# Performance work log

Measured on AMD Instinct MI355X. Metric: run time of the kernel, lower is better.

Reference implementation:

```python
import jax, jax.numpy as jnp
import numpy as np

B, C, H, W = 8, 64, 128, 128
G, DGPG = 4, 1
GD = G * DGPG          # total deformable groups = 4
COUT = 64
KH = KW = 3
K = KH * KW            # 9 kernel locations
PAD = STR = DIL = 1
HO, WO = 128, 128      # same padding, stride 1
OFFSET_SCALE = 1.0
CDG = C // GD          # channels per deformable group = 16
CPG = C // G           # input channels per conv group = 16
KOFF = 7
POFF = 3


def dwconv7(x, w, b):
    # depthwise 7x7 conv, groups == channels; w: [C,1,7,7]
    y = jax.lax.conv_general_dilated(
        x, w, window_strides=(1, 1), padding=[(POFF, POFF), (POFF, POFF)],
        feature_group_count=C, dimension_numbers=('NCHW', 'OIHW', 'NCHW'))
    return y + b[None, :, None, None]


def gn1(x, g, b):
    # GroupNorm with a single group: normalize over (C,H,W) per sample
    m = x.mean(axis=(1, 2, 3), keepdims=True)
    v = x.var(axis=(1, 2, 3), keepdims=True)
    return (x - m) * jax.lax.rsqrt(v + 1e-5) * g[None, :, None, None] + b[None, :, None, None]


def pw(x, w, b):
    # 1x1 conv; w: [O, C]
    return jnp.einsum('bchw,oc->bohw', x, w) + b[None, :, None, None]


def setup_inputs() -> dict:
    key = jax.random.key(0)
    ks = jax.random.split(key, 8)
    s = 0.02
    return {
        'x': jax.random.normal(ks[0], (B, C, H, W), jnp.float32),
        'w_dw_off': jax.random.normal(ks[1], (C, 1, KOFF, KOFF), jnp.float32) * s,
        'b_dw_off': jnp.zeros((C,), jnp.float32),
        'gn_off_g': jnp.ones((C,), jnp.float32),
        'gn_off_b': jnp.zeros((C,), jnp.float32),
        'w_pw_off': jax.random.normal(ks[2], (GD * K * 2, C), jnp.float32) * s,
        'b_pw_off': jnp.zeros((GD * K * 2,), jnp.float32),
        'w_dw_m': jax.random.normal(ks[3], (C, 1, KOFF, KOFF), jnp.float32) * s,
        'b_dw_m': jnp.zeros((C,), jnp.float32),
        'gn_m_g': jnp.ones((C,), jnp.float32),
        'gn_m_b': jnp.zeros((C,), jnp.float32),
        'w_pw_m': jax.random.normal(ks[4], (GD * K, C), jnp.float32) * s,
        'b_pw_m': jnp.zeros((GD * K,), jnp.float32),
        'weight': jax.random.normal(ks[5], (COUT, CPG, KH, KW), jnp.float32) * s,
        'bias': jax.random.normal(ks[6], (COUT,), jnp.float32) * s,
    }


def _deform_conv(x, offset, mask, weight, bias):
    # offset: [B, GD, K, 2, HO, WO] (y, x); mask: [B, GD, K, HO, WO] (softmaxed)
    ky, kx = jnp.meshgrid(jnp.arange(KH), jnp.arange(KW), indexing='ij')
    ky = ky.reshape(K).astype(x.dtype)
    kx = kx.reshape(K).astype(x.dtype)
    oy = jnp.arange(HO, dtype=x.dtype)
    ox = jnp.arange(WO, dtype=x.dtype)
    base_y = oy[None, :] * STR - PAD + ky[:, None] * DIL   # [K, HO]
    base_x = ox[None, :] * STR - PAD + kx[:, None] * DIL   # [K, WO]
    py = base_y[None, None, :, :, None] + offset[:, :, :, 0] * OFFSET_SCALE  # [B,GD,K,HO,WO]
    px = base_x[None, None, :, None, :] + offset[:, :, :, 1] * OFFSET_SCALE

    x_flat = x.reshape(B, GD, CDG, H * W)
    y0 = jnp.floor(py)
    x0 = jnp.floor(px)
    wy = py - y0
    wx = px - x0

    def gather(yi, xi):
        valid = ((yi >= 0) & (yi < H) & (xi >= 0) & (xi < W)).astype(x.dtype)
        yc = jnp.clip(yi, 0, H - 1).astype(jnp.int32)
        xc = jnp.clip(xi, 0, W - 1).astype(jnp.int32)
        idx = (yc * W + xc).reshape(B, GD, 1, K * HO * WO)
        v = jnp.take_along_axis(x_flat, idx, axis=3).reshape(B, GD, CDG, K, HO, WO)
        return v * valid[:, :, None]

    v = (gather(y0, x0) * ((1 - wy) * (1 - wx))[:, :, None]
         + gather(y0, x0 + 1) * ((1 - wy) * wx)[:, :, None]
         + gather(y0 + 1, x0) * (wy * (1 - wx))[:, :, None]
         + gather(y0 + 1, x0 + 1) * (wy * wx)[:, :, None])
    v = v * mask[:, :, None]                               # modulated samples
    v = v.reshape(B, G, CPG, K, HO, WO)
    wg = weight.reshape(G, COUT // G, CPG, K)
    out = jnp.einsum('bgckhw,gock->bgohw', v, wg).reshape(B, COUT, HO, WO)
    return out + bias[None, :, None, None]


def reference(x, w_dw_off, b_dw_off, gn_off_g, gn_off_b, w_pw_off, b_pw_off,
              w_dw_m, b_dw_m, gn_m_g, gn_m_b, w_pw_m, b_pw_m, weight, bias):
    off = pw(gn1(dwconv7(x, w_dw_off, b_dw_off), gn_off_g, gn_off_b), w_pw_off, b_pw_off)
    m = pw(gn1(dwconv7(x, w_dw_m, b_dw_m), gn_m_g, gn_m_b), w_pw_m, b_pw_m)
    offset = off.reshape(B, GD, K, 2, HO, WO)
    mask = jax.nn.softmax(m.reshape(B, GD, K, HO, WO), axis=2)  # attn over kernel points
    return _deform_conv(x, offset, mask, weight, bias)
```

## Files before the change

kernel.cpp:

```cpp
#include <hip/hip_runtime.h>
#include <hip/hip_fp16.h>
#include <math.h>

#define HW     16384
#define IMG_H  128
#define IMG_W  128

typedef _Float16 f16x2 __attribute__((ext_vector_type(2)));
typedef __fp16 fp16v2 __attribute__((ext_vector_type(2)));
typedef _Float16 f16x4 __attribute__((ext_vector_type(4)));
typedef float f32x4 __attribute__((ext_vector_type(4)));

#define OFF_T2    ((size_t)0)
#define OFF_XT    ((size_t)8388608)
#define OFF_WT    ((size_t)12582912)
#define OFF_PART  ((size_t)12599040)
#define OFF_AD    ((size_t)12631808)
#define OFF_WB    ((size_t)19711744)
#define OFF_WDW2  ((size_t)19716352)
#define OFF_WPK   ((size_t)19719936)
#define OFF_DC    ((size_t)19775232)

__global__ void k_prep(const float* __restrict__ wpw_off,
                       const float* __restrict__ wpw_m,
                       const float* __restrict__ wdef,
                       const float* __restrict__ wdwo,
                       const float* __restrict__ wdwm,
                       float* __restrict__ ws) {
    int i = blockIdx.x * 256 + threadIdx.x;
    if (i < 6912) {
        int c = i / 108, o = i % 108;
        ws[OFF_WT + i] = (o < 72) ? wpw_off[o * 64 + c] : wpw_m[(o - 72) * 64 + c];
    } else if (i < 9216) {
        int j = i - 6912;
        int lane = j & 63;
        int gt = j >> 6;
        int tap = gt % 9, g = gt / 9;
        int oc = lane & 15, qh = lane >> 4;
        union { ushort h[4]; uint2 u; } pk;
#pragma unroll
        for (int jj = 0; jj < 4; ++jj) {
            float wv = wdef[((g * 16 + oc) * 16 + (4 * qh + jj)) * 9 + tap];
            pk.h[jj] = __half_as_ushort(__float2half(wv));
        }
        ((uint2*)(ws + OFF_WB))[j] = pk.u;
    } else if (i < 12800) {
        int j = i - 9216;
        int q = j & 3;
        int r = j >> 2;
        int dy = r % 7;
        int cv = (r / 7) & 1;
        int c = r / 14;
        const float* src = cv ? wdwm : wdwo;
        int dx0 = q * 2;
        float w0 = src[c * 49 + dy * 7 + dx0];
        float w1 = (dx0 + 1 < 7) ? src[c * 49 + dy * 7 + dx0 + 1] : 0.f;
        union { __half h[2]; uint u; } pk;
        pk.h[0] = __float2half(w0);
        pk.h[1] = __float2half(w1);
        ((uint*)(ws + OFF_WDW2))[j] = pk.u;
    }
}

__global__ __launch_bounds__(256) void k_trans(const float* __restrict__ x,
                                               __half* __restrict__ xT) {
    int n = blockIdx.x * 256 + threadIdx.x;
    int p = n & (HW - 1);
    int bg = n >> 14;
    const float* src = x + (size_t)bg * 16 * HW + p;
    union { __half2 h2[8]; uint4 u[2]; } pk;
#pragma unroll
    for (int i = 0; i < 8; ++i) {
        float a = src[(size_t)(2 * i) * HW];
        float bq = src[(size_t)(2 * i + 1) * HW];
        pk.h2[i] = __halves2half2(__float2half(a), __float2half(bq));
    }
    uint4* dst = (uint4*)(xT + (size_t)n * 16);
    dst[0] = pk.u[0];
    dst[1] = pk.u[1];
}

__global__ __launch_bounds__(256) void k_dw(const float* __restrict__ x,
                                            const float* __restrict__ bdwo,
                                            const float* __restrict__ bdwm,
                                            const uint* __restrict__ wdw2,
                                            uint2* __restrict__ t2p,
                                            float* __restrict__ partial) {
    int bid = blockIdx.x;
    int b = bid >> 9;
    int c2 = (bid >> 4) & 31;
    int stripe = (bid & 15) * 8;
    int t = threadIdx.x;
    int cb = t & 31;
    int row = stripe + (t >> 5);
    int c0 = c2 * 2;

    float vo[2][4], vm[2][4];
    float s1o = 0.f, s2o = 0.f, s1m = 0.f, s2m = 0.f;
    union CV { fp16v2 v; f16x2 h; };
    union WU { uint u; f16x2 h; };

#pragma unroll
    for (int ch = 0; ch < 2; ++ch) {
        int c = c0 + ch;
        const float4* pl = (const float4*)(x + ((size_t)(b * 64 + c)) * HW);
        const uint* wp = wdw2 + c * 56;
        float acco[4] = {0.f, 0.f, 0.f, 0.f};
        float accm[4] = {0.f, 0.f, 0.f, 0.f};
#pragma unroll
        for (int dy = 0; dy < 7; ++dy) {
            int iy = row - 3 + dy;
            if (iy >= 0 && iy < IMG_H) {
                const float4* prow = pl + iy * 32;
                float4 f4 = prow[cb];
                float4 f4m = prow[cb == 0 ? 0 : cb - 1];
                float4 f4p = prow[cb == 31 ? 31 : cb + 1];
                bool le = (cb == 0), re = (cb == 31);
                float v[11];
                v[0] = le ? 0.f : f4m.y;
                v[1] = le ? 0.f : f4m.z;
                v[2] = le ? 0.f : f4m.w;
                v[3] = f4.x; v[4] = f4.y; v[5] = f4.z; v[6] = f4.w;
                v[7] = re ? 0.f : f4p.x;
                v[8] = re ? 0.f : f4p.y;
                v[9] = re ? 0.f : f4p.z;
                v[10] = re ? 0.f : f4p.w;
                f16x2 hp[10];
#pragma unroll
                for (int d = 0; d < 10; ++d) {
                    CV cv;
                    cv.v = __builtin_amdgcn_cvt_pkrtz(v[d], v[d + 1]);
                    hp[d] = cv.h;
                }
#pragma unroll
                for (int cc = 0; cc < 4; ++cc) {
                    WU w0, w1, w2, w3, u0, u1, u2, u3;
                    w0.u = wp[dy * 4 + 0]; w1.u = wp[dy * 4 + 1];
                    w2.u = wp[dy * 4 + 2]; w3.u = wp[dy * 4 + 3];
                    u0.u = wp[28 + dy * 4 + 0]; u1.u = wp[28 + dy * 4 + 1];
                    u2.u = wp[28 + dy * 4 + 2]; u3.u = wp[28 + dy * 4 + 3];
                    float ao = acco[cc], am = accm[cc];
                    ao = __builtin_amdgcn_fdot2(hp[cc],     w0.h, ao, false);
                    ao = __builtin_amdgcn_fdot2(hp[cc + 2], w1.h, ao, false);
                    ao = __builtin_amdgcn_fdot2(hp[cc + 4], w2.h, ao, false);
                    ao = __builtin_amdgcn_fdot2(hp[cc + 6], w3.h, ao, false);
                    am = __builtin_amdgcn_fdot2(hp[cc],     u0.h, am, false);
                    am = __builtin_amdgcn_fdot2(hp[cc + 2], u1.h, am, false);
                    am = __builtin_amdgcn_fdot2(hp[cc + 4], u2.h, am, false);
                    am = __builtin_amdgcn_fdot2(hp[cc + 6], u3.h, am, false);
                    acco[cc] = ao; accm[cc] = am;
                }
            }
        }
        float bo = bdwo[c], bm = bdwm[c];
#pragma unroll
        for (int cc = 0; cc < 4; ++cc) {
            float o_ = acco[cc] + bo, m_ = accm[cc] + bm;
            vo[ch][cc] = o_; vm[ch][cc] = m_;
            s1o += o_; s2o += o_ * o_; s1m += m_; s2m += m_ * m_;
        }
    }

    union { uint2 u2[4]; uint4 u4[2]; } ot;
#pragma unroll
    for (int cc = 0; cc < 4; ++cc) {
        ot.u2[cc].x = (uint)__half_as_ushort(__float2half(vo[0][cc])) |
                      ((uint)__half_as_ushort(__float2half(vo[1][cc])) << 16);
        ot.u2[cc].y = (uint)__half_as_ushort(__float2half(vm[0][cc])) |
                      ((uint)__half_as_ushort(__float2half(vm[1][cc])) << 16);
    }
    uint4* dst = (uint4*)(t2p + ((size_t)(b * 32 + c2) * HW + row * IMG_W + cb * 4));
    dst[0] = ot.u4[0];
    dst[1] = ot.u4[1];

#pragma unroll
    for (int d = 32; d; d >>= 1) {
        s1o += __shfl_down(s1o, d);
        s2o += __shfl_down(s2o, d);
        s1m += __shfl_down(s1m, d);
        s2m += __shfl_down(s2m, d);
    }
    __shared__ float red[4][4];
    if ((t & 63) == 0) {
        int w = t >> 6;
        red[w][0] = s1o; red[w][1] = s2o; red[w][2] = s1m; red[w][3] = s2m;
    }
    __syncthreads();
    if (t < 4) {
        float v = red[0][t] + red[1][t] + red[2][t] + red[3][t];
        partial[(size_t)bid * 4 + t] = v;
    }
}

__global__ __launch_bounds__(256) void k_fin(const float* __restrict__ partial,
                      const float* __restrict__ gog, const float* __restrict__ gob,
                      const float* __restrict__ gmg, const float* __restrict__ gmb,
                      float* __restrict__ ad) {
    int b = blockIdx.x, t = threadIdx.x;
    const float4* pp = (const float4*)partial + (size_t)b * 512;
    float4 s = make_float4(0.f, 0.f, 0.f, 0.f);
#pragma unroll
    for (int i = 0; i < 2; ++i) {
        float4 v = pp[t + i * 256];
        s.x += v.x; s.y += v.y; s.z += v.z; s.w += v.w;
    }
#pragma unroll
    for (int d = 32; d; d >>= 1) {
        s.x += __shfl_down(s.x, d);
        s.y += __shfl_down(s.y, d);
        s.z += __shfl_down(s.z, d);
        s.w += __shfl_down(s.w, d);
    }
    __shared__ float red[4][4];
    if ((t & 63) == 0) {
        int w = t >> 6;
        red[w][0] = s.x; red[w][1] = s.y; red[w][2] = s.z; red[w][3] = s.w;
    }
    __syncthreads();
    if (t < 64) {
        float s1o = red[0][0] + red[1][0] + red[2][0] + red[3][0];
        float s2o = red[0][1] + red[1][1] + red[2][1] + red[3][1];
        float s1m = red[0][2] + red[1][2] + red[2][2] + red[3][2];
        float s2m = red[0][3] + red[1][3] + red[2][3] + red[3][3];
        int c = t;
        const float invN = 1.f / 1048576.f;
        float m_o = s1o * invN;
        float v_o = s2o * invN - m_o * m_o;
        float i_o = rsqrtf(v_o + 1e-5f);
        float m_m = s1m * invN;
        float v_m = s2m * invN - m_m * m_m;
        float i_m = rsqrtf(v_m + 1e-5f);
        float a_o = i_o * gog[c];
        float d_o = gob[c] - m_o * a_o;
        float a_m = i_m * gmg[c];
        float d_m = gmb[c] - m_m * a_m;
        ((float4*)ad)[b * 64 + c] = make_float4(a_o, d_o, a_m, d_m);
    }
}

__global__ __launch_bounds__(256) void k_fold(const float* __restrict__ wT,
                                              const float* __restrict__ ad,
                                              const float* __restrict__ bpo,
                                              const float* __restrict__ bpm,
                                              uint* __restrict__ wpk,
                                              float* __restrict__ dconst) {
    int b = blockIdx.x, t = threadIdx.x;
    const float* adb = ad + b * 256;
    for (int i = t; i < 3456; i += 256) {
        int o27 = i % 27;
        int c2 = (i / 27) & 31;
        int g = i / (27 * 32);
        int c0 = c2 * 2, c1 = c0 + 1;
        float w0, w1;
        if (o27 < 18) {
            int o = g * 18 + o27;
            w0 = adb[c0 * 4 + 0] * wT[c0 * 108 + o];
            w1 = adb[c1 * 4 + 0] * wT[c1 * 108 + o];
        } else {
            int o = 72 + g * 9 + (o27 - 18);
            w0 = adb[c0 * 4 + 2] * wT[c0 * 108 + o];
            w1 = adb[c1 * 4 + 2] * wT[c1 * 108 + o];
        }
        wpk[(size_t)b * 3456 + i] =
            (uint)__half_as_ushort(__float2half(w0)) |
            ((uint)__half_as_ushort(__float2half(w1)) << 16);
    }
    if (t < 108) {
        float s = (t < 72) ? bpo[t] : bpm[t - 72];
        for (int c = 0; c < 64; ++c) {
            float d = (t < 72) ? adb[c * 4 + 1] : adb[c * 4 + 3];
            s = fmaf(d, wT[c * 108 + t], s);
        }
        dconst[b * 108 + t] = s;
    }
}

__global__ __launch_bounds__(256, 4) void k_gthf(const uint2* __restrict__ t2p,
                                                 const uint* __restrict__ wpk,
                                                 const float* __restrict__ dconst,
                                                 const __half* __restrict__ xT,
                                                 const uint2* __restrict__ wb,
                                                 const float* __restrict__ bias,
                                                 float* __restrict__ out) {
    __shared__ union SMem {
        struct {
            uint4 xsA[506];
            uint4 xsB[506];
            uint4 shv[768];
        } s;
        float shout[4864];
    } sm;

    int tid = threadIdx.x;
    int bid = blockIdx.x;
    int bg = bid >> 6;
    int tile = bid & 63;
    int tr = tile >> 3, tc = tile & 7;
    int r0 = tr * 16, c0 = tc * 16;
    int g = bg & 3, b = bg >> 2;
    int wr0 = r0 - 3, wc0 = c0 - 3;

    const __half* xg = xT + (size_t)bg * HW * 16;

#pragma unroll
    for (int it = 0; it < 2; ++it) {
        int idx = tid + it * 256;
        if (idx < 484) {
            int ly = idx / 22, lx = idx - ly * 22;
            int sr = wr0 + ly; sr = sr < 0 ? 0 : (sr > 127 ? 127 : sr);
            int sc = wc0 + lx; sc = sc < 0 ? 0 : (sc > 127 ? 127 : sc);
            const uint4* src = (const uint4*)(xg + (size_t)(sr * IMG_W + sc) * 16);
            sm.s.xsA[ly * 23 + lx] = src[0];
            sm.s.xsB[ly * 23 + lx] = src[1];
        }
    }

    int row = r0 + (tid >> 4), col = c0 + (tid & 15);
    int p = row * IMG_W + col;
    int lane = tid & 63, wv = tid >> 6;
    int m_idx = lane & 15, q_idx = lane >> 4;

    const float* dc = dconst + b * 108;
    float facc[18], macc[9];
#pragma unroll
    for (int o = 0; o < 18; ++o) facc[o] = dc[g * 18 + o];
#pragma unroll
    for (int o = 0; o < 9; ++o) macc[o] = dc[72 + g * 9 + o];

    const uint2* tp = t2p + (size_t)b * 32 * HW + p;
    const uint* wgp = wpk + ((size_t)(b * 4 + g)) * 32 * 27;
    union WU { uint u; f16x2 h; };
#pragma unroll 8
    for (int c2 = 0; c2 < 32; ++c2) {
        uint2 pk = tp[(size_t)c2 * HW];
        WU ho, hm;
        ho.u = pk.x; hm.u = pk.y;
        const uint* wr = wgp + c2 * 27;
#pragma unroll
        for (int o = 0; o < 18; ++o) {
            WU w; w.u = wr[o];
            facc[o] = __builtin_amdgcn_fdot2(ho.h, w.h, facc[o], false);
        }
#pragma unroll
        for (int o = 0; o < 9; ++o) {
            WU w; w.u = wr[18 + o];
            macc[o] = __builtin_amdgcn_fdot2(hm.h, w.h, macc[o], false);
        }
    }
    {
        float mx = macc[0];
#pragma unroll
        for (int k = 1; k < 9; ++k) mx = fmaxf(mx, macc[k]);
        float s = 0.f;
#pragma unroll
        for (int k = 0; k < 9; ++k) {
            float e = __expf(macc[k] - mx);
            macc[k] = e;
            s += e;
        }
        float inv = 1.f / s;
#pragma unroll
        for (int k = 0; k < 9; ++k) macc[k] *= inv;
    }

    const uint2* wbp = wb + (size_t)(g * 9) * 64 + lane;
    f16x4 bfr[9];
    union BU { uint2 u; f16x4 h; };
#pragma unroll
    for (int k = 0; k < 9; ++k) { BU t; t.u = wbp[k * 64]; bfr[k] = t.h; }

    __syncthreads();

    uint4* shvw = sm.s.shv + tid * 3;
    const _Float16* shvh = (const _Float16*)sm.s.shv;

    f32x4 acc[4];
#pragma unroll
    for (int s = 0; s < 4; ++s) acc[s] = (f32x4){0.f, 0.f, 0.f, 0.f};

#pragma unroll
    for (int k = 0; k < 9; ++k) {
        float mk = macc[k];
        float py = (float)(row + k / 3 - 1) + facc[k * 2 + 0];
        float px = (float)(col + k % 3 - 1) + facc[k * 2 + 1];
        float y0f = floorf(py), x0f = floorf(px);
        float wy = py - y0f, wx = px - x0f;
        int iy0 = (int)y0f, ix0 = (int)x0f;
        int iy1 = iy0 + 1, ix1 = ix0 + 1;
        float fy0 = (iy0 >= 0 && iy0 < IMG_H) ? (1.f - wy) : 0.f;
        float fy1 = (iy1 >= 0 && iy1 < IMG_H) ? wy : 0.f;
        float fx0 = (ix0 >= 0 && ix0 < IMG_W) ? (1.f - wx) : 0.f;
        float fx1 = (ix1 >= 0 && ix1 < IMG_W) ? wx : 0.f;
        __half2 f00h = __float2half2_rn(fy0 * fx0 * mk);
        __half2 f01h = __float2half2_rn(fy0 * fx1 * mk);
        __half2 f10h = __float2half2_rn(fy1 * fx0 * mk);
        __half2 f11h = __float2half2_rn(fy1 * fx1 * mk);
        int ly0 = iy0 - wr0; ly0 = ly0 < 0 ? 0 : (ly0 > 21 ? 21 : ly0);
        int ly1 = iy1 - wr0; ly1 = ly1 < 0 ? 0 : (ly1 > 21 ? 21 : ly1);
        int lx0 = ix0 - wc0; lx0 = lx0 < 0 ? 0 : (lx0 > 21 ? 21 : lx0);
        int lx1 = ix1 - wc0; lx1 = lx1 < 0 ? 0 : (lx1 > 21 ? 21 : lx1);
        int i00 = ly0 * 23 + lx0, i01 = ly0 * 23 + lx1;
        int i10 = ly1 * 23 + lx0, i11 = ly1 * 23 + lx1;
        union Q8 { uint4 u[2]; __half2 h2[8]; };
        Q8 q00, q01, q10, q11;
        q00.u[0] = sm.s.xsA[i00]; q00.u[1] = sm.s.xsB[i00];
        q01.u[0] = sm.s.xsA[i01]; q01.u[1] = sm.s.xsB[i01];
        q10.u[0] = sm.s.xsA[i10]; q10.u[1] = sm.s.xsB[i10];
        q11.u[0] = sm.s.xsA[i11]; q11.u[1] = sm.s.xsB[i11];
        union V8 { __half2 h2[4]; uint4 u; };
        V8 pa, pb;
#pragma unroll
        for (int i = 0; i < 4; ++i) {
            __half2 vh = __hmul2(f00h, q00.h2[i]);
            vh = __hfma2(f01h, q01.h2[i], vh);
            vh = __hfma2(f10h, q10.h2[i], vh);
            vh = __hfma2(f11h, q11.h2[i], vh);
            pa.h2[i] = vh;
        }
#pragma unroll
        for (int i = 4; i < 8; ++i) {
            __half2 vh = __hmul2(f00h, q00.h2[i]);
            vh = __hfma2(f01h, q01.h2[i], vh);
            vh = __hfma2(f10h, q10.h2[i], vh);
            vh = __hfma2(f11h, q11.h2[i], vh);
            pb.h2[i - 4] = vh;
        }
        shvw[0] = pa.u;
        shvw[1] = pb.u;
#pragma unroll
        for (int s = 0; s < 4; ++s) {
            f16x4 af = *(const f16x4*)(shvh +
                        ((size_t)wv * 64 + s * 16 + m_idx) * 24 + q_idx * 4);
            acc[s] = __builtin_amdgcn_mfma_f32_16x16x16f16(af, bfr[k], acc[s], 0, 0, 0);
        }
    }

    __syncthreads();

#pragma unroll
    for (int s = 0; s < 4; ++s)
#pragma unroll
        for (int j = 0; j < 4; ++j)
            sm.shout[(wv * 64 + s * 16 + 4 * q_idx + j) * 19 + m_idx] = acc[s][j];

    float* outp = out + ((size_t)b * 64 + g * 16) * HW + p;
#pragma unroll
    for (int o = 0; o < 16; ++o)
        outp[(size_t)o * HW] = sm.shout[tid * 19 + o] + bias[g * 16 + o];
}

extern "C" void kernel_launch(void* const* d_in, const int* in_sizes, int n_in,
                              void* d_out, int out_size, void* d_ws, size_t ws_size,
                              hipStream_t stream) {
    const float* x        = (const float*)d_in[0];
    const float* w_dw_off = (const float*)d_in[1];
    const float* b_dw_off = (const float*)d_in[2];
    const float* gn_off_g = (const float*)d_in[3];
    const float* gn_off_b = (const float*)d_in[4];
    const float* w_pw_off = (const float*)d_in[5];
    const float* b_pw_off = (const float*)d_in[6];
    const float* w_dw_m   = (const float*)d_in[7];
    const float* b_dw_m   = (const float*)d_in[8];
    const float* gn_m_g   = (const float*)d_in[9];
    const float* gn_m_b   = (const float*)d_in[10];
    const float* w_pw_m   = (const float*)d_in[11];
    const float* b_pw_m   = (const float*)d_in[12];
    const float* weight   = (const float*)d_in[13];
    const float* bias     = (const float*)d_in[14];

    float* ws = (float*)d_ws;
    uint2* t2p    = (uint2*)(ws + OFF_T2);
    __half* xT    = (__half*)(ws + OFF_XT);
    float* wT     = ws + OFF_WT;
    float* part   = ws + OFF_PART;
    float* adb    = ws + OFF_AD;
    const uint2* wb = (const uint2*)(ws + OFF_WB);
    const uint* wdw2 = (const uint*)(ws + OFF_WDW2);
    uint* wpk     = (uint*)(ws + OFF_WPK);
    float* dconst = ws + OFF_DC;

    k_prep<<<50, 256, 0, stream>>>(w_pw_off, w_pw_m, weight, w_dw_off, w_dw_m, ws);
    k_trans<<<2048, 256, 0, stream>>>(x, xT);
    k_dw<<<4096, 256, 0, stream>>>(x, b_dw_off, b_dw_m, wdw2, t2p, part);
    k_fin<<<8, 256, 0, stream>>>(part, gn_off_g, gn_off_b, gn_m_g, gn_m_b, adb);
    k_fold<<<8, 256, 0, stream>>>(wT, adb, b_pw_off, b_pw_m, wpk, dconst);
    k_gthf<<<2048, 256, 0, stream>>>(t2p, wpk, dconst, xT, wb, bias, (float*)d_out);
}
```

Baseline: 103.6 us.

## Compute offset/mask pointwise projection with MFMA instead of per-thread fdot2

Replaces the per-pixel fdot2 loop that produced the 18 offset and 9 mask logits with 16x16x16 fp16 MFMA tiles. k_fold now packs the GN-folded pointwise weights directly into MFMA B-fragment layout, with zero padding up to 32 and 16 outputs. The activations are staged through a per-wave LDS slab to form A fragments, and the accumulators are transposed back through LDS to per-pixel registers. This cuts the scalar ALU dot-product work in the fused gather kernel, at the cost of more LDS traffic and footprint. The offsets are also rounded to fp16 before the bias is added, which costs some accuracy.

```diff
diff --git a/kernel.cpp b/kernel.cpp
--- a/kernel.cpp
+++ b/kernel.cpp
@@ -18,8 +18,9 @@
 #define OFF_AD    ((size_t)12631808)
 #define OFF_WB    ((size_t)19711744)
 #define OFF_WDW2  ((size_t)19716352)
-#define OFF_WPK   ((size_t)19719936)
-#define OFF_DC    ((size_t)19775232)
+#define OFF_WBO   ((size_t)19719936)
+#define OFF_WBM   ((size_t)19752704)
+#define OFF_DC    ((size_t)19769088)
 
 __global__ void k_prep(const float* __restrict__ wpw_off,
                        const float* __restrict__ wpw_m,
@@ -242,28 +243,39 @@
                                               const float* __restrict__ ad,
                                               const float* __restrict__ bpo,
                                               const float* __restrict__ bpm,
-                                              uint* __restrict__ wpk,
+                                              uint2* __restrict__ wbo,
+                                              uint2* __restrict__ wbm,
                                               float* __restrict__ dconst) {
     int b = blockIdx.x, t = threadIdx.x;
     const float* adb = ad + b * 256;
-    for (int i = t; i < 3456; i += 256) {
-        int o27 = i % 27;
-        int c2 = (i / 27) & 31;
-        int g = i / (27 * 32);
-        int c0 = c2 * 2, c1 = c0 + 1;
-        float w0, w1;
-        if (o27 < 18) {
-            int o = g * 18 + o27;
-            w0 = adb[c0 * 4 + 0] * wT[c0 * 108 + o];
-            w1 = adb[c1 * 4 + 0] * wT[c1 * 108 + o];
-        } else {
-            int o = 72 + g * 9 + (o27 - 18);
-            w0 = adb[c0 * 4 + 2] * wT[c0 * 108 + o];
-            w1 = adb[c1 * 4 + 2] * wT[c1 * 108 + o];
-        }
-        wpk[(size_t)b * 3456 + i] =
-            (uint)__half_as_ushort(__float2half(w0)) |
-            ((uint)__half_as_ushort(__float2half(w1)) << 16);
+    for (int i = t; i < 2048; i += 256) {
+        int lane = i & 63;
+        int f = i >> 6;
+        int g = f >> 3, kk = (f >> 1) & 3, nf = f & 1;
+        int n = lane & 15, q = lane >> 4;
+        int out = nf * 16 + n;
+        union { ushort h[4]; uint2 u; } pk;
+#pragma unroll
+        for (int jj = 0; jj < 4; ++jj) {
+            int ch = kk * 16 + 4 * q + jj;
+            float w = (out < 18) ? adb[ch * 4 + 0] * wT[ch * 108 + g * 18 + out] : 0.f;
+            pk.h[jj] = __half_as_ushort(__float2half(w));
+        }
+        wbo[((size_t)(b * 4) + g) * 8 * 64 + (size_t)(kk * 2 + nf) * 64 + lane] = pk.u;
+    }
+    for (int i = t; i < 1024; i += 256) {
+        int lane = i & 63;
+        int f = i >> 6;
+        int g = f >> 2, kk = f & 3;
+        int n = lane & 15, q = lane >> 4;
+        union { ushort h[4]; uint2 u; } pk;
+#pragma unroll
+        for (int jj = 0; jj < 4; ++jj) {
+            int ch = kk * 16 + 4 * q + jj;
+            float w = (n < 9) ? adb[ch * 4 + 2] * wT[ch * 108 + 72 + g * 9 + n] : 0.f;
+            pk.h[jj] = __half_as_ushort(__float2half(w));
+        }
+        wbm[((size_t)(b * 4) + g) * 4 * 64 + (size_t)kk * 64 + lane] = pk.u;
     }
     if (t < 108) {
         float s = (t < 72) ? bpo[t] : bpm[t - 72];
@@ -276,7 +288,8 @@
 }
 
 __global__ __launch_bounds__(256, 4) void k_gthf(const uint2* __restrict__ t2p,
-                                                 const uint* __restrict__ wpk,
+                                                 const uint2* __restrict__ wbo,
+                                                 const uint2* __restrict__ wbm,
                                                  const float* __restrict__ dconst,
                                                  const __half* __restrict__ xT,
                                                  const uint2* __restrict__ wb,
@@ -286,7 +299,7 @@
         struct {
             uint4 xsA[506];
             uint4 xsB[506];
-            uint4 shv[768];
+            uint  slab[5120];
         } s;
         float shout[4864];
     } sm;
@@ -320,133 +333,187 @@
     int lane = tid & 63, wv = tid >> 6;
     int m_idx = lane & 15, q_idx = lane >> 4;
 
+    union BU { uint2 u; f16x4 h; };
+
+    const uint2* wboP = wbo + ((size_t)(b * 4) + g) * 8 * 64 + lane;
+    const uint2* wbmP = wbm + ((size_t)(b * 4) + g) * 4 * 64 + lane;
+    f16x4 bO[8], bM[4];
+#pragma unroll
+    for (int i = 0; i < 8; ++i) { BU t; t.u = wboP[i * 64]; bO[i] = t.h; }
+#pragma unroll
+    for (int i = 0; i < 4; ++i) { BU t; t.u = wbmP[i * 64]; bM[i] = t.h; }
+
+    const uint2* wbp = wb + (size_t)(g * 9) * 64 + lane;
+    f16x4 bfr[9];
+#pragma unroll
+    for (int k = 0; k < 9; ++k) { BU t; t.u = wbp[k * 64]; bfr[k] = t.h; }
+
+    uint* aslab = sm.s.slab + wv * 1280;
+    const uint2* tp = t2p + (size_t)b * 32 * HW + p;
+
+    f32x4 accO0[4], accO1[4], accM[4];
+#pragma unroll
+    for (int s = 0; s < 4; ++s) {
+        accO0[s] = (f32x4){0.f, 0.f, 0.f, 0.f};
+        accO1[s] = (f32x4){0.f, 0.f, 0.f, 0.f};
+        accM[s]  = (f32x4){0.f, 0.f, 0.f, 0.f};
+    }
+
+#pragma unroll
+    for (int kk = 0; kk < 4; ++kk) {
+        uint2 v[8];
+#pragma unroll
+        for (int j = 0; j < 8; ++j) v[j] = tp[(size_t)(kk * 8 + j) * HW];
+        uint* rowp = aslab + lane * 20;
+        ((uint4*)rowp)[0] = make_uint4(v[0].x, v[1].x, v[2].x, v[3].x);
+        ((uint4*)rowp)[1] = make_uint4(v[4].x, v[5].x, v[6].x, v[7].x);
+        ((uint4*)(rowp + 8))[0] = make_uint4(v[0].y, v[1].y, v[2].y, v[3].y);
+        ((uint4*)(rowp + 8))[1] = make_uint4(v[4].y, v[5].y, v[6].y, v[7].y);
+#pragma unroll
+        for (int s = 0; s < 4; ++s) {
+            const uint* pr = aslab + (s * 16 + m_idx) * 20 + 2 * q_idx;
+            BU ao, am;
+            ao.u = *(const uint2*)pr;
+            am.u = *(const uint2*)(pr + 8);
+            accO0[s] = __builtin_amdgcn_mfma_f32_16x16x16f16(ao.h, bO[kk * 2 + 0], accO0[s], 0, 0, 0);
+            accO1[s] = __builtin_amdgcn_mfma_f32_16x16x16f16(ao.h, bO[kk * 2 + 1], accO1[s], 0, 0, 0);
+            accM[s]  = __builtin_amdgcn_mfma_f32_16x16x16f16(am.h, bM[kk], accM[s], 0, 0, 0);
+        }
+    }
+
     const float* dc = dconst + b * 108;
-    float facc[18], macc[9];
-#pragma unroll
-    for (int o = 0; o < 18; ++o) facc[o] = dc[g * 18 + o];
-#pragma unroll
-    for (int o = 0; o < 9; ++o) macc[o] = dc[72 + g * 9 + o];
-
-    const uint2* tp = t2p + (size_t)b * 32 * HW + p;
-    const uint* wgp = wpk + ((size_t)(b * 4 + g)) * 32 * 27;
-    union WU { uint u; f16x2 h; };
-#pragma unroll 8
-    for (int c2 = 0; c2 < 32; ++c2) {
-        uint2 pk = tp[(size_t)c2 * HW];
-        WU ho, hm;
-        ho.u = pk.x; hm.u = pk.y;
-        const uint* wr = wgp + c2 * 27;
-#pragma unroll
-        for (int o = 0; o < 18; ++o) {
-            WU w; w.u = wr[o];
-            facc[o] = __builtin_amdgcn_fdot2(ho.h, w.h, facc[o], false);
-        }
-#pragma unroll
-        for (int o = 0; o < 9; ++o) {
-            WU w; w.u = wr[18 + o];
-            macc[o] = __builtin_amdgcn_fdot2(hm.h, w.h, macc[o], false);
-        }
-    }
+
+#pragma unroll
+    for (int s = 0; s < 4; ++s)
+#pragma unroll
+        for (int j = 0; j < 4; ++j) {
+            int px = s * 16 + 4 * q_idx + j;
+            union { __half2 h2; uint u; } pk;
+            pk.h2 = __halves2half2(__float2half(accO0[s][j]),
+                                   __float2half(accO1[s][j]));
+            aslab[px * 20 + m_idx] = pk.u;
+        }
+    float facc[18];
     {
+        const uint4* dr = (const uint4*)(aslab + lane * 20);
+        uint4 d0 = dr[0], d1 = dr[1], d2 = dr[2], d3 = dr[3];
+        uint du[16] = {d0.x, d0.y, d0.z, d0.w, d1.x, d1.y, d1.z, d1.w,
+                       d2.x, d2.y, d2.z, d2.w, d3.x, d3.y, d3.z, d3.w};
+        union { uint u; __half2 h2; } cv;
+#pragma unroll
+        for (int i = 0; i < 16; ++i) {
+            cv.u = du[i];
+            float2 f = __half22float2(cv.h2);
+            facc[i] = f.x + dc[g * 18 + i];
+            if (i < 2) facc[16 + i] = f.y + dc[g * 18 + 16 + i];
+        }
+    }
+
+    {
+        float* fsl = (float*)aslab;
+#pragma unroll
+        for (int s = 0; s < 4; ++s)
+#pragma unroll
+            for (int j = 0; j < 4; ++j) {
+                int px = s * 16 + 4 * q_idx + j;
+                fsl[px * 20 + m_idx] = accM[s][j];
+            }
+        float macc[9];
+#pragma unroll
+        for (int k = 0; k < 9; ++k) macc[k] = fsl[lane * 20 + k] + dc[72 + g * 9 + k];
         float mx = macc[0];
 #pragma unroll
         for (int k = 1; k < 9; ++k) mx = fmaxf(mx, macc[k]);
-        float s = 0.f;
+        float ssum = 0.f;
 #pragma unroll
         for (int k = 0; k < 9; ++k) {
             float e = __expf(macc[k] - mx);
             macc[k] = e;
-            s += e;
-        }
-        float inv = 1.f / s;
-#pragma unroll
-        for (int k = 0; k < 9; ++k) macc[k] *= inv;
-    }
-
-    const uint2* wbp = wb + (size_t)(g * 9) * 64 + lane;
-    f16x4 bfr[9];
-    union BU { uint2 u; f16x4 h; };
-#pragma unroll
-    for (int k = 0; k < 9; ++k) { BU t; t.u = wbp[k * 64]; bfr[k] = t.h; }
-
-    __syncthreads();
-
-    uint4* shvw = sm.s.shv + tid * 3;
-    const _Float16* shvh = (const _Float16*)sm.s.shv;
-
-    f32x4 acc[4];
-#pragma unroll
-    for (int s = 0; s < 4; ++s) acc[s] = (f32x4){0.f, 0.f, 0.f, 0.f};
-
-#pragma unroll
-    for (int k = 0; k < 9; ++k) {
-        float mk = macc[k];
-        float py = (float)(row + k / 3 - 1) + facc[k * 2 + 0];
-        float px = (float)(col + k % 3 - 1) + facc[k * 2 + 1];
-        float y0f = floorf(py), x0f = floorf(px);
-        float wy = py - y0f, wx = px - x0f;
-        int iy0 = (int)y0f, ix0 = (int)x0f;
-        int iy1 = iy0 + 1, ix1 = ix0 + 1;
-        float fy0 = (iy0 >= 0 && iy0 < IMG_H) ? (1.f - wy) : 0.f;
-        float fy1 = (iy1 >= 0 && iy1 < IMG_H) ? wy : 0.f;
-        float fx0 = (ix0 >= 0 && ix0 < IMG_W) ? (1.f - wx) : 0.f;
-        float fx1 = (ix1 >= 0 && ix1 < IMG_W) ? wx : 0.f;
-        __half2 f00h = __float2half2_rn(fy0 * fx0 * mk);
-        __half2 f01h = __float2half2_rn(fy0 * fx1 * mk);
-        __half2 f10h = __float2half2_rn(fy1 * fx0 * mk);
-        __half2 f11h = __float2half2_rn(fy1 * fx1 * mk);
-        int ly0 = iy0 - wr0; ly0 = ly0 < 0 ? 0 : (ly0 > 21 ? 21 : ly0);
-        int ly1 = iy1 - wr0; ly1 = ly1 < 0 ? 0 : (ly1 > 21 ? 21 : ly1);
-        int lx0 = ix0 - wc0; lx0 = lx0 < 0 ? 0 : (lx0 > 21 ? 21 : lx0);
-        int lx1 = ix1 - wc0; lx1 = lx1 < 0 ? 0 : (lx1 > 21 ? 21 : lx1);
-        int i00 = ly0 * 23 + lx0, i01 = ly0 * 23 + lx1;
-        int i10 = ly1 * 23 + lx0, i11 = ly1 * 23 + lx1;
-        union Q8 { uint4 u[2]; __half2 h2[8]; };
-        Q8 q00, q01, q10, q11;
-        q00.u[0] = sm.s.xsA[i00]; q00.u[1] = sm.s.xsB[i00];
-        q01.u[0] = sm.s.xsA[i01]; q01.u[1] = sm.s.xsB[i01];
-        q10.u[0] = sm.s.xsA[i10]; q10.u[1] = sm.s.xsB[i10];
-        q11.u[0] = sm.s.xsA[i11]; q11.u[1] = sm.s.xsB[i11];
-        union V8 { __half2 h2[4]; uint4 u; };
-        V8 pa, pb;
-#pragma unroll
-        for (int i = 0; i < 4; ++i) {
-            __half2 vh = __hmul2(f00h, q00.h2[i]);
-            vh = __hfma2(f01h, q01.h2[i], vh);
-            vh = __hfma2(f10h, q10.h2[i], vh);
-            vh = __hfma2(f11h, q11.h2[i], vh);
-            pa.h2[i] = vh;
-        }
-#pragma unroll
-        for (int i = 4; i < 8; ++i) {
-            __half2 vh = __hmul2(f00h, q00.h2[i]);
-            vh = __hfma2(f01h, q01.h2[i], vh);
-            vh = __hfma2(f10h, q10.h2[i], vh);
-            vh = __hfma2(f11h, q11.h2[i], vh);
-            pb.h2[i - 4] = vh;
-        }
-        shvw[0] = pa.u;
-        shvw[1] = pb.u;
-#pragma unroll
-        for (int s = 0; s < 4; ++s) {
-            f16x4 af = *(const f16x4*)(shvh +
-                        ((size_t)wv * 64 + s * 16 + m_idx) * 24 + q_idx * 4);
-            acc[s] = __builtin_amdgcn_mfma_f32_16x16x16f16(af, bfr[k], acc[s], 0, 0, 0);
-        }
-    }
-
-    __syncthreads();
-
-#pragma unroll
-    for (int s = 0; s < 4; ++s)
-#pragma unroll
-        for (int j = 0; j < 4; ++j)
-            sm.shout[(wv * 64 + s * 16 + 4 * q_idx + j) * 19 + m_idx] = acc[s][j];
-
-    float* outp = out + ((size_t)b * 64 + g * 16) * HW + p;
-#pragma unroll
-    for (int o = 0; o < 16; ++o)
-        outp[(size_t)o * HW] = sm.shout[tid * 19 + o] + bias[g * 16 + o];
+            ssum += e;
+        }
+        float inv = 1.f / ssum;
+#pragma unroll
+        for (int k = 0; k < 9; ++k) facc[k] = facc[k], macc[k] *= inv;
+
+        __syncthreads();
+
+        uint4* shvw = (uint4*)aslab + lane * 3;
+        const _Float16* shvh = (const _Float16*)aslab;
+
+        f32x4 acc[4];
+#pragma unroll
+        for (int s = 0; s < 4; ++s) acc[s] = (f32x4){0.f, 0.f, 0.f, 0.f};
+
+#pragma unroll
+        for (int k = 0; k < 9; ++k) {
+            float mk = macc[k];
+            float py = (float)(row + k / 3 - 1) + facc[k * 2 + 0];
+            float px = (float)(col + k % 3 - 1) + facc[k * 2 + 1];
+            float y0f = floorf(py), x0f = floorf(px);
+            float wy = py - y0f, wx = px - x0f;
+            int iy0 = (int)y0f, ix0 = (int)x0f;
+            int iy1 = iy0 + 1, ix1 = ix0 + 1;
+            float fy0 = (iy0 >= 0 && iy0 < IMG_H) ? (1.f - wy) : 0.f;
+            float fy1 = (iy1 >= 0 && iy1 < IMG_H) ? wy : 0.f;
+            float fx0 = (ix0 >= 0 && ix0 < IMG_W) ? (1.f - wx) : 0.f;
+            float fx1 = (ix1 >= 0 && ix1 < IMG_W) ? wx : 0.f;
+            __half2 f00h = __float2half2_rn(fy0 * fx0 * mk);
+            __half2 f01h = __float2half2_rn(fy0 * fx1 * mk);
+            __half2 f10h = __float2half2_rn(fy1 * fx0 * mk);
+            __half2 f11h = __float2half2_rn(fy1 * fx1 * mk);
+            int ly0 = iy0 - wr0; ly0 = ly0 < 0 ? 0 : (ly0 > 21 ? 21 : ly0);
+            int ly1 = iy1 - wr0; ly1 = ly1 < 0 ? 0 : (ly1 > 21 ? 21 : ly1);
+            int lx0 = ix0 - wc0; lx0 = lx0 < 0 ? 0 : (lx0 > 21 ? 21 : lx0);
+            int lx1 = ix1 - wc0; lx1 = lx1 < 0 ? 0 : (lx1 > 21 ? 21 : lx1);
+            int i00 = ly0 * 23 + lx0, i01 = ly0 * 23 + lx1;
+            int i10 = ly1 * 23 + lx0, i11 = ly1 * 23 + lx1;
+            union Q8 { uint4 u[2]; __half2 h2[8]; };
+            Q8 q00, q01, q10, q11;
+            q00.u[0] = sm.s.xsA[i00]; q00.u[1] = sm.s.xsB[i00];
+            q01.u[0] = sm.s.xsA[i01]; q01.u[1] = sm.s.xsB[i01];
+            q10.u[0] = sm.s.xsA[i10]; q10.u[1] = sm.s.xsB[i10];
+            q11.u[0] = sm.s.xsA[i11]; q11.u[1] = sm.s.xsB[i11];
+            union V8 { __half2 h2[4]; uint4 u; };
+            V8 pa, pb;
+#pragma unroll
+            for (int i = 0; i < 4; ++i) {
+                __half2 vh = __hmul2(f00h, q00.h2[i]);
+                vh = __hfma2(f01h, q01.h2[i], vh);
+                vh = __hfma2(f10h, q10.h2[i], vh);
+                vh = __hfma2(f11h, q11.h2[i], vh);
+                pa.h2[i] = vh;
+            }
+#pragma unroll
+            for (int i = 4; i < 8; ++i) {
+                __half2 vh = __hmul2(f00h, q00.h2[i]);
+                vh = __hfma2(f01h, q01.h2[i], vh);
+                vh = __hfma2(f10h, q10.h2[i], vh);
+                vh = __hfma2(f11h, q11.h2[i], vh);
+                pb.h2[i - 4] = vh;
+            }
+            shvw[0] = pa.u;
+            shvw[1] = pb.u;
+#pragma unroll
+            for (int s = 0; s < 4; ++s) {
+                f16x4 af = *(const f16x4*)(shvh +
+                            ((size_t)(s * 16 + m_idx)) * 24 + q_idx * 4);
+                acc[s] = __builtin_amdgcn_mfma_f32_16x16x16f16(af, bfr[k], acc[s], 0, 0, 0);
+            }
+        }
+
+        __syncthreads();
+
+#pragma unroll
+        for (int s = 0; s < 4; ++s)
+#pragma unroll
+            for (int j = 0; j < 4; ++j)
+                sm.shout[(wv * 64 + s * 16 + 4 * q_idx + j) * 19 + m_idx] = acc[s][j];
+
+        float* outp = out + ((size_t)b * 64 + g * 16) * HW + p;
+#pragma unroll
+        for (int o = 0; o < 16; ++o)
+            outp[(size_t)o * HW] = sm.shout[tid * 19 + o] + bias[g * 16 + o];
+    }
 }
 
 extern "C" void kernel_launch(void* const* d_in, const int* in_sizes, int n_in,
@@ -476,13 +543,14 @@
     float* adb    = ws + OFF_AD;
     const uint2* wb = (const uint2*)(ws + OFF_WB);
     const uint* wdw2 = (const uint*)(ws + OFF_WDW2);
-    uint* wpk     = (uint*)(ws + OFF_WPK);
+    uint2* wbo    = (uint2*)(ws + OFF_WBO);
+    uint2* wbm    = (uint2*)(ws + OFF_WBM);
     float* dconst = ws + OFF_DC;
 
     k_prep<<<50, 256, 0, stream>>>(w_pw_off, w_pw_m, weight, w_dw_off, w_dw_m, ws);
     k_trans<<<2048, 256, 0, stream>>>(x, xT);
     k_dw<<<4096, 256, 0, stream>>>(x, b_dw_off, b_dw_m, wdw2, t2p, part);
     k_fin<<<8, 256, 0, stream>>>(part, gn_off_g, gn_off_b, gn_m_g, gn_m_b, adb);
-    k_fold<<<8, 256, 0, stream>>>(wT, adb, b_pw_off, b_pw_m, wpk, dconst);
-    k_gthf<<<2048, 256, 0, stream>>>(t2p, wpk, dconst, xT, wb, bias, (float*)d_out);
-}
+    k_fold<<<8, 256, 0, stream>>>(wT, adb, b_pw_off, b_pw_m, wbo, wbm, dconst);
+    k_gthf<<<2048, 256, 0, stream>>>(t2p, wbo, wbm, dconst, xT, wb, bias, (float*)d_out);
+}
```

New measurement: 100.7 us. 1.03x faster.
